# Optimization experiments

Measured on AMD Instinct MI355X. Metric: run time of the kernel, lower is better.

## Reference

```python
import jax, jax.numpy as jnp
import numpy as np

B, T, D, H = 4096, 512, 25, 25
NUM_LAYERS = 3


def setup_inputs() -> dict:
    key = jax.random.key(0)
    ks = jax.random.split(key, 9)
    s = 1.0 / np.sqrt(H)  # torch LSTM/Linear default init scale
    return {
        "x": jax.random.normal(ks[0], (B, T, D), dtype=jnp.float32),
        "Wih": jax.random.uniform(ks[1], (NUM_LAYERS, 4 * H, D), minval=-s, maxval=s),
        "Whh": jax.random.uniform(ks[2], (NUM_LAYERS, 4 * H, H), minval=-s, maxval=s),
        "bih": jax.random.uniform(ks[3], (NUM_LAYERS, 4 * H), minval=-s, maxval=s),
        "bhh": jax.random.uniform(ks[4], (NUM_LAYERS, 4 * H), minval=-s, maxval=s),
        "W1": jax.random.uniform(ks[5], (16, H), minval=-s, maxval=s),
        "b1": jax.random.uniform(ks[6], (16,), minval=-s, maxval=s),
        "W2": jax.random.uniform(ks[7], (14, 16), minval=-0.25, maxval=0.25),
        "b2": jax.random.uniform(ks[8], (14,), minval=-0.25, maxval=0.25),
    }


def _lstm_layer(x, Wih, Whh, b):
    """Single LSTM layer, batch_first. x: [B,T,Din] -> hs: [B,T,H].
    Torch gate order: i, f, g, o."""
    # Precompute input contribution for all timesteps at once: [B,T,4H]
    xg = jnp.einsum('btd,gd->btg', x, Wih) + b

    def step(carry, xg_t):
        h, c = carry
        g = xg_t + h @ Whh.T  # [B,4H]
        i, f, gg, o = jnp.split(g, 4, axis=-1)
        c = jax.nn.sigmoid(f) * c + jax.nn.sigmoid(i) * jnp.tanh(gg)
        h = jax.nn.sigmoid(o) * jnp.tanh(c)
        return (h, c), h

    h0 = jnp.zeros((x.shape[0], H), x.dtype)
    (_, _), hs = jax.lax.scan(step, (h0, h0), jnp.swapaxes(xg, 0, 1))  # [T,B,H]
    return jnp.swapaxes(hs, 0, 1)


def reference(x, Wih, Whh, bih, bhh, W1, b1, W2, b2):
    h = x
    for l in range(NUM_LAYERS):  # eval mode: inter-layer dropout disabled
        h = _lstm_layer(h, Wih[l], Whh[l], bih[l] + bhh[l])
    last = h[:, -1, :]                       # [B,H]
    out = jax.nn.relu(last @ W1.T + b1)      # [B,16]
    return jax.nn.softmax(out @ W2.T + b2, axis=1)  # [B,14]
```

## Files before the change

### kernel.cpp

```cpp
#include <hip/hip_runtime.h>


#define NBATCH 4096
#define NT     512
#define ND     25
#define NG     100
#define NL     3

__device__ __forceinline__ float sigf(float x) {
    return __builtin_amdgcn_rcpf(1.0f + __expf(-x));
}
__device__ __forceinline__ float tanhfast(float x) {
    float s = sigf(x + x);
    return s + s - 1.0f;
}

__global__ __launch_bounds__(256, 3)
void lstm3(const float* __restrict__ xin,
           const float* __restrict__ Wih,
           const float* __restrict__ Whh,
           const float* __restrict__ bih,
           const float* __restrict__ bhh,
           const float* __restrict__ W1,
           const float* __restrict__ b1,
           const float* __restrict__ W2,
           const float* __restrict__ b2,
           float* __restrict__ out,
           float* __restrict__ ws)
{
    __shared__ __align__(16) float xh[2][2][56];
    __shared__ float act[2][2][112];

    const int wid  = threadIdx.x >> 6;
    const int lane = threadIdx.x & 63;
    const int wb   = wid >> 1;
    const int role = wid & 1;
    const int b    = (blockIdx.x << 1) + wb;

    const int lrow = (lane < 50) ? lane : 49;
    float* const myxh = xh[wb][role];

    float w[52];
    w[50] = 0.f; w[51] = 0.f;

    for (int l = 0; l < NL; ++l) {
        const int row = l * NG + role * 50 + lrow;
        const float* wihp = Wih + row * ND;
        const float* whhp = Whh + row * ND;
#pragma unroll
        for (int d = 0; d < 25; ++d) { w[d] = wihp[d]; w[25 + d] = whhp[d]; }
        const float bias = bih[row] + bhh[row];

        const float* src = (l == 0) ? (xin + (size_t)b * NT * ND)
                                    : (ws  + (size_t)b * NT * ND);
        float* wsrow = ws + (size_t)b * NT * ND;

        float c = 0.f;
        if (lane < 25)                    myxh[lane] = src[lane];
        else if (lane < 56)               myxh[lane] = 0.f;
        float xv_next = (lane < 25) ? src[ND + lane] : 0.f;
        __syncthreads();

        for (int t = 0; t < NT; ++t) {
            const int p = t & 1;
            float a0 = bias, a1 = 0.f, a2 = 0.f, a3 = 0.f;
#pragma unroll
            for (int c4 = 0; c4 < 13; ++c4) {
                const float4 v = *(const float4*)&myxh[c4 * 4];
                a0 = fmaf(w[c4 * 4 + 0], v.x, a0);
                a1 = fmaf(w[c4 * 4 + 1], v.y, a1);
                a2 = fmaf(w[c4 * 4 + 2], v.z, a2);
                a3 = fmaf(w[c4 * 4 + 3], v.w, a3);
            }
            const float acc = (a0 + a1) + (a2 + a3);

            float a;
            if (role == 0) a = sigf(acc);
            else           a = (lane < 25) ? tanhfast(acc)
                                           : sigf(acc);
            if (lane < 50) act[wb][p][role * 56 + lane] = a;
            __syncthreads();

            if (lane < 25) {
                const float ig = act[wb][p][lane];
                const float fg = act[wb][p][25 + lane];
                const float gg = act[wb][p][56 + lane];
                const float og = act[wb][p][81 + lane];
                c = fmaf(fg, c, ig * gg);
                const float h = og * tanhfast(c);
                myxh[25 + lane] = h;
                myxh[lane]      = xv_next;
                if (role == 0 && l < 2) wsrow[t * ND + lane] = h;
                if (t + 2 < NT) xv_next = src[(t + 2) * ND + lane];
            }
        }
    }

    if (role == 0) {
        float* sc = act[wb][0];
        if (lane < 16) {
            float u = b1[lane];
#pragma unroll
            for (int d = 0; d < 25; ++d) u = fmaf(W1[lane * 25 + d], myxh[25 + d], u);
            sc[lane] = fmaxf(u, 0.f);
        }
        if (lane < 14) {
            float lg = b2[lane];
#pragma unroll
            for (int r = 0; r < 16; ++r) lg = fmaf(W2[lane * 16 + r], sc[r], lg);
            sc[32 + lane] = lg;
        }
        if (lane < 14) {
            float m = -1e30f;
#pragma unroll
            for (int j = 0; j < 14; ++j) m = fmaxf(m, sc[32 + j]);
            float sum = 0.f;
#pragma unroll
            for (int j = 0; j < 14; ++j) sum += __expf(sc[32 + j] - m);
            out[b * 14 + lane] = __expf(sc[32 + lane] - m) / sum;
        }
    }
}

extern "C" void kernel_launch(void* const* d_in, const int* in_sizes, int n_in,
                              void* d_out, int out_size, void* d_ws, size_t ws_size,
                              hipStream_t stream)
{
    const float* x   = (const float*)d_in[0];
    const float* Wih = (const float*)d_in[1];
    const float* Whh = (const float*)d_in[2];
    const float* bih = (const float*)d_in[3];
    const float* bhh = (const float*)d_in[4];
    const float* W1  = (const float*)d_in[5];
    const float* b1  = (const float*)d_in[6];
    const float* W2  = (const float*)d_in[7];
    const float* b2  = (const float*)d_in[8];
    float* outp = (float*)d_out;
    float* ws   = (float*)d_ws;

    dim3 grid(NBATCH / 2), block(256);
    hipLaunchKernelGGL(lstm3, grid, block, 0, stream,
                       x, Wih, Whh, bih, bhh, W1, b1, W2, b2, outp, ws);
}
```

Measured before the change: 1.907 ms.

## Compute cell update redundantly in all lanes and broadcast h via readlane

Every wave now keeps the hidden state in registers and broadcasts it through readlane instead of shared memory. The four gate activations are packed per unit into a float4 so all lanes can run the cell update redundantly, which removes the second barrier in each timestep and leaves one raw s_barrier. Gate activations are merged into a single exp2/rcp expression chosen per lane, and the head also uses readlane. The costs are many more scalar readlane operations, redundant cell math in both waves, and occupancy lowered to 2 in launch bounds.

```diff
diff --git a/kernel.cpp b/kernel.cpp
--- a/kernel.cpp
+++ b/kernel.cpp
@@ -1,22 +1,31 @@
 #include <hip/hip_runtime.h>
 
 
-#define NBATCH 4096
-#define NT     512
-#define ND     25
-#define NG     100
-#define NL     3
+#define NT 512
+#define ND 25
+#define NL 3
 
-__device__ __forceinline__ float sigf(float x) {
-    return __builtin_amdgcn_rcpf(1.0f + __expf(-x));
+__device__ __forceinline__ float exp2f_(float x) { return __builtin_amdgcn_exp2f(x); }
+__device__ __forceinline__ float tanhfast(float x) {
+    float s = __builtin_amdgcn_rcpf(1.f + exp2f_(-2.885390082f * x));
+    return fmaf(2.f, s, -1.f);
 }
-__device__ __forceinline__ float tanhfast(float x) {
-    float s = sigf(x + x);
-    return s + s - 1.0f;
+__device__ __forceinline__ float rdlane(float v, int i) {
+    return __uint_as_float(__builtin_amdgcn_readlane(__float_as_uint(v), i));
 }
 
-__global__ __launch_bounds__(256, 3)
-void lstm3(const float* __restrict__ xin,
+#define L28(M) M(0) M(1) M(2) M(3) M(4) M(5) M(6) M(7) M(8) M(9) M(10) M(11) \
+               M(12) M(13) M(14) M(15) M(16) M(17) M(18) M(19) M(20) M(21) \
+               M(22) M(23) M(24) M(25) M(26) M(27)
+
+#define WDECL(i) float wi##i, wh##i;
+#define WLOAD(i) wi##i = ((i) < ND) ? wihp[(i) < ND ? (i) : 0] : 0.f; \
+                 wh##i = ((i) < ND) ? whhp[(i) < ND ? (i) : 0] : 0.f;
+
+#define HT(i, A) A = fmaf(wh##i, rdlane(hreg, i), A);
+
+__global__ __launch_bounds__(256, 2)
+void lstm5(const float* __restrict__ xin,
            const float* __restrict__ Wih,
            const float* __restrict__ Whh,
            const float* __restrict__ bih,
@@ -28,8 +37,8 @@
            float* __restrict__ out,
            float* __restrict__ ws)
 {
-    __shared__ __align__(16) float xh[2][2][56];
-    __shared__ float act[2][2][112];
+    __shared__ __align__(16) float xb[2][2][28];
+    __shared__ __align__(16) float act4[2][2][25][4];
 
     const int wid  = threadIdx.x >> 6;
     const int lane = threadIdx.x & 63;
@@ -38,87 +47,123 @@
     const int b    = (blockIdx.x << 1) + wb;
 
     const int lrow = (lane < 50) ? lane : 49;
-    float* const myxh = xh[wb][role];
 
-    float w[52];
-    w[50] = 0.f; w[51] = 0.f;
+    const int ul   = (lrow >= ND) ? lrow - ND : lrow;
+    const int slot = role * 2 + (lrow >= ND ? 1 : 0);
+    float* const actw0 = &act4[wb][0][ul][slot];
+    float* const actw1 = &act4[wb][1][ul][slot];
+    const int ur = (lane < ND) ? lane : ND - 1;
+    const float4* const actr0 = (const float4*)&act4[wb][0][ur][0];
+    const float4* const actr1 = (const float4*)&act4[wb][1][ur][0];
+    const float4* const xr0 = (const float4*)&xb[wb][0][0];
+    const float4* const xr1 = (const float4*)&xb[wb][1][0];
+    float* const xw0 = &xb[wb][0][lane < ND ? lane : 0];
+    float* const xw1 = &xb[wb][1][lane < ND ? lane : 0];
+
+    const bool  isg    = (role == 1) && (lane < ND);
+    const float emul   = isg ? -2.885390082f : -1.442695041f;
+    const float ascale = isg ?  2.0f : 1.0f;
+    const float abias  = isg ? -1.0f : 0.0f;
+
+    L28(WDECL)
+
+    float hreg = 0.f;
 
     for (int l = 0; l < NL; ++l) {
-        const int row = l * NG + role * 50 + lrow;
+        const int row = l * 100 + role * 50 + lrow;
         const float* wihp = Wih + row * ND;
         const float* whhp = Whh + row * ND;
-#pragma unroll
-        for (int d = 0; d < 25; ++d) { w[d] = wihp[d]; w[25 + d] = whhp[d]; }
+        L28(WLOAD)
         const float bias = bih[row] + bhh[row];
 
         const float* src = (l == 0) ? (xin + (size_t)b * NT * ND)
                                     : (ws  + (size_t)b * NT * ND);
         float* wsrow = ws + (size_t)b * NT * ND;
 
+        __syncthreads();
+
+        if (role == 0) {
+            if (lane < ND)       xb[wb][0][lane] = src[lane];
+            else if (lane < 28) { xb[wb][0][lane] = 0.f; xb[wb][1][lane] = 0.f; }
+        }
         float c = 0.f;
-        if (lane < 25)                    myxh[lane] = src[lane];
-        else if (lane < 56)               myxh[lane] = 0.f;
-        float xv_next = (lane < 25) ? src[ND + lane] : 0.f;
+        hreg = 0.f;
+        float xnext = (role == 0 && lane < ND) ? src[ND + lane] : 0.f;
         __syncthreads();
 
         for (int t = 0; t < NT; ++t) {
             const int p = t & 1;
+            const float4* const xr = p ? xr1 : xr0;
+
+            const float4 v0 = xr[0], v1 = xr[1], v2 = xr[2], v3 = xr[3];
+            const float4 v4 = xr[4], v5 = xr[5], v6 = xr[6];
             float a0 = bias, a1 = 0.f, a2 = 0.f, a3 = 0.f;
-#pragma unroll
-            for (int c4 = 0; c4 < 13; ++c4) {
-                const float4 v = *(const float4*)&myxh[c4 * 4];
-                a0 = fmaf(w[c4 * 4 + 0], v.x, a0);
-                a1 = fmaf(w[c4 * 4 + 1], v.y, a1);
-                a2 = fmaf(w[c4 * 4 + 2], v.z, a2);
-                a3 = fmaf(w[c4 * 4 + 3], v.w, a3);
-            }
-            const float acc = (a0 + a1) + (a2 + a3);
+            a0 = fmaf(wi0,  v0.x, a0); a1 = fmaf(wi1,  v0.y, a1);
+            a2 = fmaf(wi2,  v0.z, a2); a3 = fmaf(wi3,  v0.w, a3);
+            a0 = fmaf(wi4,  v1.x, a0); a1 = fmaf(wi5,  v1.y, a1);
+            a2 = fmaf(wi6,  v1.z, a2); a3 = fmaf(wi7,  v1.w, a3);
+            a0 = fmaf(wi8,  v2.x, a0); a1 = fmaf(wi9,  v2.y, a1);
+            a2 = fmaf(wi10, v2.z, a2); a3 = fmaf(wi11, v2.w, a3);
+            a0 = fmaf(wi12, v3.x, a0); a1 = fmaf(wi13, v3.y, a1);
+            a2 = fmaf(wi14, v3.z, a2); a3 = fmaf(wi15, v3.w, a3);
+            a0 = fmaf(wi16, v4.x, a0); a1 = fmaf(wi17, v4.y, a1);
+            a2 = fmaf(wi18, v4.z, a2); a3 = fmaf(wi19, v4.w, a3);
+            a0 = fmaf(wi20, v5.x, a0); a1 = fmaf(wi21, v5.y, a1);
+            a2 = fmaf(wi22, v5.z, a2); a3 = fmaf(wi23, v5.w, a3);
+            a0 = fmaf(wi24, v6.x, a0); a1 = fmaf(wi25, v6.y, a1);
+            a2 = fmaf(wi26, v6.z, a2); a3 = fmaf(wi27, v6.w, a3);
 
-            float a;
-            if (role == 0) a = sigf(acc);
-            else           a = (lane < 25) ? tanhfast(acc)
-                                           : sigf(acc);
-            if (lane < 50) act[wb][p][role * 56 + lane] = a;
-            __syncthreads();
+            float b0 = 0.f, b1r = 0.f, b2r = 0.f, b3 = 0.f;
+            HT(0,  b0) HT(1,  b1r) HT(2,  b2r) HT(3,  b3)
+            HT(4,  b0) HT(5,  b1r) HT(6,  b2r) HT(7,  b3)
+            HT(8,  b0) HT(9,  b1r) HT(10, b2r) HT(11, b3)
+            HT(12, b0) HT(13, b1r) HT(14, b2r) HT(15, b3)
+            HT(16, b0) HT(17, b1r) HT(18, b2r) HT(19, b3)
+            HT(20, b0) HT(21, b1r) HT(22, b2r) HT(23, b3)
+            HT(24, b0)
+            const float acc = ((a0 + a1) + (a2 + a3)) + ((b0 + b1r) + (b2r + b3));
 
-            if (lane < 25) {
-                const float ig = act[wb][p][lane];
-                const float fg = act[wb][p][25 + lane];
-                const float gg = act[wb][p][56 + lane];
-                const float og = act[wb][p][81 + lane];
-                c = fmaf(fg, c, ig * gg);
-                const float h = og * tanhfast(c);
-                myxh[25 + lane] = h;
-                myxh[lane]      = xv_next;
-                if (role == 0 && l < 2) wsrow[t * ND + lane] = h;
-                if (t + 2 < NT) xv_next = src[(t + 2) * ND + lane];
-            }
+            const float a = fmaf(ascale,
+                                 __builtin_amdgcn_rcpf(1.f + exp2f_(emul * acc)),
+                                 abias);
+            if (lane < 50) *(p ? actw1 : actw0) = a;
+
+            if (role == 0 && lane < ND) *(p ? xw0 : xw1) = xnext;
+            if (role == 0 && lane < ND && t + 2 < NT)
+                xnext = src[(size_t)(t + 2) * ND + lane];
+
+            asm volatile("s_waitcnt lgkmcnt(0)\n\ts_barrier" ::: "memory");
+
+            const float4 q = p ? *actr1 : *actr0;
+            c = fmaf(q.y, c, q.x * q.z);
+            hreg = q.w * tanhfast(c);
+            if (role == 0 && lane < ND && l < 2) wsrow[(size_t)t * ND + lane] = hreg;
         }
     }
 
-    if (role == 0) {
-        float* sc = act[wb][0];
-        if (lane < 16) {
-            float u = b1[lane];
+    {
+        const int hl = (lane < 16) ? lane : 15;
+        float u = b1[hl];
 #pragma unroll
-            for (int d = 0; d < 25; ++d) u = fmaf(W1[lane * 25 + d], myxh[25 + d], u);
-            sc[lane] = fmaxf(u, 0.f);
-        }
-        if (lane < 14) {
-            float lg = b2[lane];
+        for (int d = 0; d < ND; ++d)
+            u = fmaf(W1[hl * ND + d], rdlane(hreg, d), u);
+        u = fmaxf(u, 0.f);
+
+        const int cl = (lane < 14) ? lane : 13;
+        float lg = b2[cl];
 #pragma unroll
-            for (int r = 0; r < 16; ++r) lg = fmaf(W2[lane * 16 + r], sc[r], lg);
-            sc[32 + lane] = lg;
-        }
-        if (lane < 14) {
-            float m = -1e30f;
+        for (int r = 0; r < 16; ++r)
+            lg = fmaf(W2[cl * 16 + r], rdlane(u, r), lg);
+
+        float m = -1e30f;
 #pragma unroll
-            for (int j = 0; j < 14; ++j) m = fmaxf(m, sc[32 + j]);
-            float sum = 0.f;
+        for (int j = 0; j < 14; ++j) m = fmaxf(m, rdlane(lg, j));
+        float sum = 0.f;
 #pragma unroll
-            for (int j = 0; j < 14; ++j) sum += __expf(sc[32 + j] - m);
-            out[b * 14 + lane] = __expf(sc[32 + lane] - m) / sum;
-        }
+        for (int j = 0; j < 14; ++j)
+            sum += exp2f_(1.442695041f * (rdlane(lg, j) - m));
+        const float p = exp2f_(1.442695041f * (lg - m)) * __builtin_amdgcn_rcpf(sum);
+        if (role == 0 && lane < 14) out[b * 14 + lane] = p;
     }
 }
 
@@ -138,7 +183,7 @@
     float* outp = (float*)d_out;
     float* ws   = (float*)d_ws;
 
-    dim3 grid(NBATCH / 2), block(256);
-    hipLaunchKernelGGL(lstm3, grid, block, 0, stream,
+    dim3 grid(4096 / 2), block(256);
+    hipLaunchKernelGGL(lstm5, grid, block, 0, stream,
                        x, Wih, Whh, bih, bhh, W1, b1, W2, b2, outp, ws);
 }
```

After: 2.875 ms. 50.7% more time.

## Run one wavefront per sequence with packed-FMA gate dots and no block barriers

Applied to the files above, without the earlier changes.

Replaces the four-wave block, where waves split gate rows and exchanged activations through LDS with two __syncthreads per step, with a single 64-lane wavefront per batch element. Each lane computes all four gates for one hidden unit. The input half and the recurrent half of the dot product are split across the two 32-lane halves and combined with a cross-half shuffle. Dot products use v_pk_fma_f32 on paired weights, and activations use exp2/rcp intrinsics. The goal is to shorten the serial per-timestep critical path by removing barriers and the separate cell-update phase. The cost is duplicated transcendental work per lane and more weight registers.

```diff
diff --git a/kernel.cpp b/kernel.cpp
--- a/kernel.cpp
+++ b/kernel.cpp
@@ -1,124 +1,146 @@
 #include <hip/hip_runtime.h>
 
 
-#define NBATCH 4096
-#define NT     512
-#define ND     25
-#define NG     100
-#define NL     3
+typedef float f32x2 __attribute__((ext_vector_type(2)));
+typedef float f32x4 __attribute__((ext_vector_type(4)));
 
-__device__ __forceinline__ float sigf(float x) {
-    return __builtin_amdgcn_rcpf(1.0f + __expf(-x));
+#define NT 512
+#define ND 25
+
+__device__ __forceinline__ float exp2f_(float x){ return __builtin_amdgcn_exp2f(x); }
+__device__ __forceinline__ float rcpf_(float x){ return __builtin_amdgcn_rcpf(x); }
+__device__ __forceinline__ float sigf(float x){ return rcpf_(1.f + exp2f_(-1.442695041f*x)); }
+__device__ __forceinline__ float tanhf_(float x){ return fmaf(2.f, rcpf_(1.f + exp2f_(-2.885390082f*x)), -1.f); }
+__device__ __forceinline__ void pkfma(f32x2& a, f32x2 w, f32x2 v) {
+    asm("v_pk_fma_f32 %0, %1, %2, %0" : "+v"(a) : "v"(w), "v"(v));
 }
-__device__ __forceinline__ float tanhfast(float x) {
-    float s = sigf(x + x);
-    return s + s - 1.0f;
-}
+#define LO2(v) __builtin_shufflevector(v, v, 0, 1)
+#define HI2(v) __builtin_shufflevector(v, v, 2, 3)
 
-__global__ __launch_bounds__(256, 3)
-void lstm3(const float* __restrict__ xin,
-           const float* __restrict__ Wih,
-           const float* __restrict__ Whh,
-           const float* __restrict__ bih,
-           const float* __restrict__ bhh,
-           const float* __restrict__ W1,
-           const float* __restrict__ b1,
-           const float* __restrict__ W2,
-           const float* __restrict__ b2,
-           float* __restrict__ out,
-           float* __restrict__ ws)
+#define M12(F) F(0) F(1) F(2) F(3) F(4) F(5) F(6) F(7) F(8) F(9) F(10) F(11)
+
+#define WDECL(m) f32x2 wI##m, wF##m, wG##m, wO##m;
+#define WLOAD(m) wI##m = (f32x2){pI_[2*(m)], pI_[2*(m)+1]}; \
+                 wF##m = (f32x2){pF_[2*(m)], pF_[2*(m)+1]}; \
+                 wG##m = (f32x2){pG_[2*(m)], pG_[2*(m)+1]}; \
+                 wO##m = (f32x2){pO_[2*(m)], pO_[2*(m)+1]};
+
+#define DOTP(m, V) pkfma(aI, wI##m, (V)); pkfma(aF, wF##m, (V)); \
+                   pkfma(aG, wG##m, (V)); pkfma(aO, wO##m, (V));
+
+__global__ __launch_bounds__(64, 3)
+void lstm12(const float* __restrict__ xin, const float* __restrict__ Wih,
+            const float* __restrict__ Whh, const float* __restrict__ bih,
+            const float* __restrict__ bhh, const float* __restrict__ W1,
+            const float* __restrict__ b1,  const float* __restrict__ W2,
+            const float* __restrict__ b2,  float* __restrict__ out,
+            float* __restrict__ ws)
 {
-    __shared__ __align__(16) float xh[2][2][56];
-    __shared__ float act[2][2][112];
+    __shared__ __align__(16) float v[2][64];
 
-    const int wid  = threadIdx.x >> 6;
-    const int lane = threadIdx.x & 63;
-    const int wb   = wid >> 1;
-    const int role = wid & 1;
-    const int b    = (blockIdx.x << 1) + wb;
+    const int lane = threadIdx.x;
+    const int u    = lane & 31;
+    const int kh   = lane >> 5;
+    const int uc   = (u < ND) ? u : ND - 1;
+    const bool au  = (u < ND);
+    const int b    = blockIdx.x;
 
-    const int lrow = (lane < 50) ? lane : 49;
-    float* const myxh = xh[wb][role];
+    v[0][lane] = 0.f; v[1][lane] = 0.f;
 
-    float w[52];
-    w[50] = 0.f; w[51] = 0.f;
+    WDECL(0) WDECL(1) WDECL(2) WDECL(3) WDECL(4) WDECL(5) WDECL(6)
+    WDECL(7) WDECL(8) WDECL(9) WDECL(10) WDECL(11) WDECL(12)
 
-    for (int l = 0; l < NL; ++l) {
-        const int row = l * NG + role * 50 + lrow;
-        const float* wihp = Wih + row * ND;
-        const float* whhp = Whh + row * ND;
-#pragma unroll
-        for (int d = 0; d < 25; ++d) { w[d] = wihp[d]; w[25 + d] = whhp[d]; }
-        const float bias = bih[row] + bhh[row];
+    float c = 0.f, h = 0.f;
 
-        const float* src = (l == 0) ? (xin + (size_t)b * NT * ND)
-                                    : (ws  + (size_t)b * NT * ND);
-        float* wsrow = ws + (size_t)b * NT * ND;
+    for (int l = 0; l < 3; ++l) {
+        const float* Wsrc = kh ? Whh : Wih;
+        const float* pI_ = Wsrc + ((size_t)l*100 + uc     ) * ND;
+        const float* pF_ = Wsrc + ((size_t)l*100 + uc + 25) * ND;
+        const float* pG_ = Wsrc + ((size_t)l*100 + uc + 50) * ND;
+        const float* pO_ = Wsrc + ((size_t)l*100 + uc + 75) * ND;
+        M12(WLOAD)
+        wI12 = (f32x2){pI_[24], 0.f}; wF12 = (f32x2){pF_[24], 0.f};
+        wG12 = (f32x2){pG_[24], 0.f}; wO12 = (f32x2){pO_[24], 0.f};
+        const float bI = bih[l*100 + uc     ] + bhh[l*100 + uc     ];
+        const float bF = bih[l*100 + uc + 25] + bhh[l*100 + uc + 25];
+        const float bG = bih[l*100 + uc + 50] + bhh[l*100 + uc + 50];
+        const float bO = bih[l*100 + uc + 75] + bhh[l*100 + uc + 75];
 
-        float c = 0.f;
-        if (lane < 25)                    myxh[lane] = src[lane];
-        else if (lane < 56)               myxh[lane] = 0.f;
-        float xv_next = (lane < 25) ? src[ND + lane] : 0.f;
-        __syncthreads();
+        const float* src = ((l == 0) ? xin : ws) + (size_t)b * NT * ND + uc;
+        float* const wsb = ws + (size_t)b * NT * ND + u;
+        c = 0.f; h = 0.f;
+        float xa = 0.f, xb = 0.f;
+        if (kh == 0 && au) {
+            v[0][u] = src[0];
+            xa = src[ND];
+            xb = src[2*ND];
+        }
+        if (kh == 1 && au) v[0][32 + u] = 0.f;
 
         for (int t = 0; t < NT; ++t) {
             const int p = t & 1;
-            float a0 = bias, a1 = 0.f, a2 = 0.f, a3 = 0.f;
-#pragma unroll
-            for (int c4 = 0; c4 < 13; ++c4) {
-                const float4 v = *(const float4*)&myxh[c4 * 4];
-                a0 = fmaf(w[c4 * 4 + 0], v.x, a0);
-                a1 = fmaf(w[c4 * 4 + 1], v.y, a1);
-                a2 = fmaf(w[c4 * 4 + 2], v.z, a2);
-                a3 = fmaf(w[c4 * 4 + 3], v.w, a3);
+            const f32x4* const vv = (const f32x4*)&v[p][kh * 32];
+
+            f32x2 aI = {0.f,0.f}, aF = {0.f,0.f}, aG = {0.f,0.f}, aO = {0.f,0.f};
+            {
+                const f32x4 q0 = vv[0], q1 = vv[1];
+                DOTP(0, LO2(q0)) DOTP(1, HI2(q0)) DOTP(2, LO2(q1)) DOTP(3, HI2(q1))
+                const f32x4 q2 = vv[2], q3 = vv[3];
+                DOTP(4, LO2(q2)) DOTP(5, HI2(q2)) DOTP(6, LO2(q3)) DOTP(7, HI2(q3))
+                const f32x4 q4 = vv[4], q5 = vv[5], q6 = vv[6];
+                DOTP(8, LO2(q4)) DOTP(9, HI2(q4)) DOTP(10, LO2(q5)) DOTP(11, HI2(q5))
+                DOTP(12, LO2(q6))
             }
-            const float acc = (a0 + a1) + (a2 + a3);
 
-            float a;
-            if (role == 0) a = sigf(acc);
-            else           a = (lane < 25) ? tanhfast(acc)
-                                           : sigf(acc);
-            if (lane < 50) act[wb][p][role * 56 + lane] = a;
-            __syncthreads();
+            float sI = aI.x + aI.y, sF = aF.x + aF.y;
+            float sG = aG.x + aG.y, sO = aO.x + aO.y;
+            sI += __shfl_xor(sI, 32);
+            sF += __shfl_xor(sF, 32);
+            sG += __shfl_xor(sG, 32);
+            sO += __shfl_xor(sO, 32);
 
-            if (lane < 25) {
-                const float ig = act[wb][p][lane];
-                const float fg = act[wb][p][25 + lane];
-                const float gg = act[wb][p][56 + lane];
-                const float og = act[wb][p][81 + lane];
-                c = fmaf(fg, c, ig * gg);
-                const float h = og * tanhfast(c);
-                myxh[25 + lane] = h;
-                myxh[lane]      = xv_next;
-                if (role == 0 && l < 2) wsrow[t * ND + lane] = h;
-                if (t + 2 < NT) xv_next = src[(t + 2) * ND + lane];
+            const float gi = sigf(sI + bI);
+            const float gf = sigf(sF + bF);
+            const float gg = tanhf_(sG + bG);
+            const float go = sigf(sO + bO);
+            c = fmaf(gf, c, gi * gg);
+            h = go * tanhf_(c);
+
+            if (au) {
+                if (kh) {
+                    v[p^1][32 + u] = h;
+                    if (l < 2) wsb[(size_t)t * ND] = h;
+                } else {
+                    v[p^1][u] = xa;
+                    xa = xb;
+                    if (t + 3 < NT) xb = src[(size_t)(t + 3) * ND];
+                }
             }
         }
+        asm volatile("s_waitcnt vmcnt(0)" ::: "memory");
     }
 
-    if (role == 0) {
-        float* sc = act[wb][0];
-        if (lane < 16) {
-            float u = b1[lane];
+    if (lane < 16) {
+        float u1 = b1[lane];
 #pragma unroll
-            for (int d = 0; d < 25; ++d) u = fmaf(W1[lane * 25 + d], myxh[25 + d], u);
-            sc[lane] = fmaxf(u, 0.f);
-        }
-        if (lane < 14) {
-            float lg = b2[lane];
+        for (int d = 0; d < ND; ++d) u1 = fmaf(W1[lane*ND + d], v[0][32 + d], u1);
+        v[0][lane] = fmaxf(u1, 0.f);
+    }
+    if (lane < 14) {
+        float lg = b2[lane];
 #pragma unroll
-            for (int r = 0; r < 16; ++r) lg = fmaf(W2[lane * 16 + r], sc[r], lg);
-            sc[32 + lane] = lg;
-        }
-        if (lane < 14) {
-            float m = -1e30f;
+        for (int k = 0; k < 16; ++k) lg = fmaf(W2[lane*16 + k], v[0][k], lg);
+        v[1][lane] = lg;
+    }
+    if (lane < 14) {
+        float m = -1e30f;
 #pragma unroll
-            for (int j = 0; j < 14; ++j) m = fmaxf(m, sc[32 + j]);
-            float sum = 0.f;
+        for (int j = 0; j < 14; ++j) m = fmaxf(m, v[1][j]);
+        float s = 0.f;
 #pragma unroll
-            for (int j = 0; j < 14; ++j) sum += __expf(sc[32 + j] - m);
-            out[b * 14 + lane] = __expf(sc[32 + lane] - m) / sum;
-        }
+        for (int j = 0; j < 14; ++j) s += exp2f_(1.442695041f * (v[1][j] - m));
+        out[(size_t)b * 14 + lane] =
+            exp2f_(1.442695041f * (v[1][lane] - m)) * rcpf_(s);
     }
 }
 
@@ -138,7 +160,7 @@
     float* outp = (float*)d_out;
     float* ws   = (float*)d_ws;
 
-    dim3 grid(NBATCH / 2), block(256);
-    hipLaunchKernelGGL(lstm3, grid, block, 0, stream,
+    dim3 grid(4096), block(64);
+    hipLaunchKernelGGL(lstm12, grid, block, 0, stream,
                        x, Wih, Whh, bih, bhh, W1, b1, W2, b2, outp, ws);
 }
```

Measured after the change: 2.065 ms. 8.3% more time.
